# Kernel tuning notes

Hardware: AMD Instinct MI355X
Metric: run time of the kernel (lower is better)

Reference implementation:

```python
import jax, jax.numpy as jnp
import numpy as np

B, N, T, D, H, L, N_HOP = 8, 512, 64, 256, 256, 2, 1
NEG = -1e18


def setup_inputs() -> dict:
    key = jax.random.key(0)
    ks = jax.random.split(key, 16)
    sc = 0.05
    return {
        "attn_mem": jax.random.normal(ks[0], (B, N, D), jnp.float32),
        "mem_sizes": jax.random.randint(ks[1], (B,), 1, N + 1).astype(jnp.int32),
        "lstm_in": jax.random.normal(ks[2], (B, T, D), jnp.float32),
        "init_h": jax.random.uniform(ks[3], (L, H), jnp.float32, -0.01, 0.01),
        "init_c": jax.random.uniform(ks[4], (L, H), jnp.float32, -0.01, 0.01),
        "init_i": jax.random.uniform(ks[5], (D,), jnp.float32, -0.1, 0.1),
        # stacked LSTM weights (layer0 input dim D == H so stacking is valid)
        "w_ih": jax.random.normal(ks[6], (L, 4 * H, D), jnp.float32) * sc,
        "w_hh": jax.random.normal(ks[7], (L, 4 * H, H), jnp.float32) * sc,
        "b_ih": jnp.zeros((L, 4 * H), jnp.float32),
        "b_hh": jnp.zeros((L, 4 * H), jnp.float32),
        "attn_wm": jax.random.normal(ks[8], (D, H), jnp.float32) * sc,
        "attn_wq": jax.random.normal(ks[9], (H, H), jnp.float32) * sc,
        "attn_v": jax.random.uniform(ks[10], (H,), jnp.float32, -0.01, 0.01),
        "hop_wm": jax.random.normal(ks[11], (D, H), jnp.float32) * sc,
        "hop_wq": jax.random.normal(ks[12], (H, H), jnp.float32) * sc,
        "hop_v": jax.random.uniform(ks[13], (H,), jnp.float32, -0.01, 0.01),
    }


def _additive_score(feat, query, v, wq):
    # feat: [B,N,H]  query: [B,S,H]  ->  score: [B,S,N]
    q = query @ wq  # [B,S,H]
    s = jnp.tanh(feat[:, None, :, :] + q[:, :, None, :])  # [B,S,N,H] (large)
    return jnp.einsum("bsnh,h->bsn", s, v)


def _run_lstm(x, h0, c0, w_ih, w_hh, b_ih, b_hh):
    # x: [S,B,D] time-major; PyTorch gate order i,f,g,o
    n_layer = h0.shape[0]

    def step(carry, x_t):
        h, c = carry
        inp = x_t
        hs, cs = [], []
        for l in range(n_layer):
            g = inp @ w_ih[l].T + h[l] @ w_hh[l].T + b_ih[l] + b_hh[l]
            i_g, f_g, g_g, o_g = jnp.split(g, 4, axis=-1)
            c_n = jax.nn.sigmoid(f_g) * c[l] + jax.nn.sigmoid(i_g) * jnp.tanh(g_g)
            h_n = jax.nn.sigmoid(o_g) * jnp.tanh(c_n)
            hs.append(h_n)
            cs.append(c_n)
            inp = h_n
        return (jnp.stack(hs), jnp.stack(cs)), inp

    _, ys = jax.lax.scan(step, (h0, c0), x)
    return ys  # [S,B,H]


def reference(attn_mem, mem_sizes, lstm_in, init_h, init_c, init_i,
              w_ih, w_hh, b_ih, b_hh,
              attn_wm, attn_wq, attn_v, hop_wm, hop_wq, hop_v):
    bs, n_mem, _ = attn_mem.shape
    attn_feat = attn_mem @ attn_wm  # [B,N,H]
    hop_feat = attn_mem @ hop_wm    # [B,N,H]

    h0 = jnp.broadcast_to(init_h[:, None, :], (init_h.shape[0], bs, init_h.shape[1]))
    c0 = jnp.broadcast_to(init_c[:, None, :], h0.shape)
    seq = jnp.concatenate(
        [jnp.broadcast_to(init_i[None, None, :], (bs, 1, init_i.shape[0])), lstm_in],
        axis=1,
    )  # [B,T+1,D]
    query = _run_lstm(seq.transpose(1, 0, 2), h0, c0, w_ih, w_hh, b_ih, b_hh)
    query = query.transpose(1, 0, 2)  # [B,T+1,H]

    valid = jnp.arange(n_mem)[None, None, :] < mem_sizes[:, None, None]  # [B,1,N]
    for _ in range(N_HOP):
        score = _additive_score(hop_feat, query, hop_v, hop_wq)  # [B,T+1,N]
        score = jnp.where(valid, score, NEG)
        norm = jax.nn.softmax(score, axis=-1)
        query = jnp.einsum("bsn,bnh->bsh", norm, hop_feat)

    return _additive_score(attn_feat, query, attn_v, attn_wq)  # [B,T+1,N]
```

## Files before the change

kernel.cpp:

```cpp
#include <hip/hip_runtime.h>

#define BB 8
#define NN 512
#define TT 64
#define SS 65
#define DD 256
#define HH 256
#define G4 1024

__device__ __forceinline__ float fsigmoid(float x) {
    return __builtin_amdgcn_rcpf(1.f + __expf(-x));
}
__device__ __forceinline__ float ftanh(float x) {
    float e = __expf(2.f * x);
    return fmaf(-2.f, __builtin_amdgcn_rcpf(e + 1.f), 1.f);
}

__global__ void prep_kernel(const float* __restrict__ lstm_in,
                            const float* __restrict__ init_i,
                            const float* __restrict__ init_h,
                            float* __restrict__ seq,
                            unsigned long long* __restrict__ S0,
                            unsigned long long* __restrict__ S1) {
    int idx = blockIdx.x * 256 + threadIdx.x;
    if (idx < BB * SS * DD) {
        int d = idx & 255;
        int r = idx >> 8;
        int s = r % SS, b = r / SS;
        seq[idx] = (s == 0) ? init_i[d]
                            : lstm_in[((size_t)b * TT + (s - 1)) * DD + d];
    } else {
        int i = idx - BB * SS * DD;
        if (i < 2048) {
            S0[i] = (1ULL << 32) | (unsigned)__float_as_uint(init_h[i & 255]);
        } else if (i < 4096) {
            S1[i - 2048] = (1ULL << 32) | (unsigned)__float_as_uint(init_h[HH + (i & 255)]);
        } else if (i < 4096 + 65 * 2048) {
            S0[2048 + (i - 4096)] = 0ULL;
        } else {
            S1[2048 + (i - (4096 + 65 * 2048))] = 0ULL;
        }
    }
}

__global__ void __launch_bounds__(256) mega_gemm_kernel(
    const float* __restrict__ attn_mem, const float* __restrict__ attn_wm,
    const float* __restrict__ hop_wm, float* __restrict__ attn_feat,
    float* __restrict__ hop_feat, const float* __restrict__ seq,
    const float* __restrict__ w_ih, const float* __restrict__ b_ih,
    const float* __restrict__ b_hh, float* __restrict__ xg0)
{
    __shared__ float As[16][68];
    __shared__ float Bs[16][68];
    __shared__ float Bs2[16][68];
    const int tid = threadIdx.x;
    const int tm = (tid >> 4) * 4, tn = (tid & 15) * 4;
    const int arow = tid >> 2, akq = (tid & 3) << 2;

    if (blockIdx.x < 256) {
        const int bm = (blockIdx.x & 63) * 64, bn = (blockIdx.x >> 6) * 64;
        float acc1[4][4] = {}, acc2[4][4] = {};
        for (int k0 = 0; k0 < 256; k0 += 16) {
            float4 va = *(const float4*)(attn_mem + (size_t)(bm + arow) * 256 + k0 + akq);
            As[akq + 0][arow] = va.x; As[akq + 1][arow] = va.y;
            As[akq + 2][arow] = va.z; As[akq + 3][arow] = va.w;
            int kk = tid >> 4, nq = (tid & 15) << 2;
            *(float4*)&Bs[kk][nq]  = *(const float4*)(attn_wm + (size_t)(k0 + kk) * 256 + bn + nq);
            *(float4*)&Bs2[kk][nq] = *(const float4*)(hop_wm  + (size_t)(k0 + kk) * 256 + bn + nq);
            __syncthreads();
#pragma unroll
            for (int kk2 = 0; kk2 < 16; ++kk2) {
                float4 a  = *(const float4*)&As[kk2][tm];
                float4 b1 = *(const float4*)&Bs[kk2][tn];
                float4 b2 = *(const float4*)&Bs2[kk2][tn];
                float av[4] = {a.x, a.y, a.z, a.w};
                float b1v[4] = {b1.x, b1.y, b1.z, b1.w};
                float b2v[4] = {b2.x, b2.y, b2.z, b2.w};
#pragma unroll
                for (int i = 0; i < 4; ++i)
#pragma unroll
                    for (int jj = 0; jj < 4; ++jj) {
                        acc1[i][jj] = fmaf(av[i], b1v[jj], acc1[i][jj]);
                        acc2[i][jj] = fmaf(av[i], b2v[jj], acc2[i][jj]);
                    }
            }
            __syncthreads();
        }
#pragma unroll
        for (int i = 0; i < 4; ++i) {
            int m = bm + tm + i;
            *(float4*)(attn_feat + (size_t)m * 256 + bn + tn) =
                make_float4(acc1[i][0], acc1[i][1], acc1[i][2], acc1[i][3]);
            *(float4*)(hop_feat + (size_t)m * 256 + bn + tn) =
                make_float4(acc2[i][0], acc2[i][1], acc2[i][2], acc2[i][3]);
        }
    } else {
        const int blk2 = blockIdx.x - 256;
        const int bm = (blk2 % 9) * 64, bn = (blk2 / 9) * 64;
        float acc[4][4] = {};
        for (int k0 = 0; k0 < 256; k0 += 16) {
            {
                int m = bm + arow;
                float4 v = make_float4(0.f, 0.f, 0.f, 0.f);
                if (m < 520) v = *(const float4*)(seq + (size_t)m * 256 + k0 + akq);
                As[akq + 0][arow] = v.x; As[akq + 1][arow] = v.y;
                As[akq + 2][arow] = v.z; As[akq + 3][arow] = v.w;
            }
            {
                int n = bn + arow;
                float4 v = *(const float4*)(w_ih + (size_t)n * 256 + k0 + akq);
                Bs[akq + 0][n - bn] = v.x; Bs[akq + 1][n - bn] = v.y;
                Bs[akq + 2][n - bn] = v.z; Bs[akq + 3][n - bn] = v.w;
            }
            __syncthreads();
#pragma unroll
            for (int kk2 = 0; kk2 < 16; ++kk2) {
                float4 a = *(const float4*)&As[kk2][tm];
                float4 b = *(const float4*)&Bs[kk2][tn];
                float av[4] = {a.x, a.y, a.z, a.w};
                float bv[4] = {b.x, b.y, b.z, b.w};
#pragma unroll
                for (int i = 0; i < 4; ++i)
#pragma unroll
                    for (int jj = 0; jj < 4; ++jj)
                        acc[i][jj] = fmaf(av[i], bv[jj], acc[i][jj]);
            }
            __syncthreads();
        }
        float bad[4];
#pragma unroll
        for (int jj = 0; jj < 4; ++jj)
            bad[jj] = b_ih[bn + tn + jj] + b_hh[bn + tn + jj];
#pragma unroll
        for (int i = 0; i < 4; ++i) {
            int m = bm + tm + i;
            if (m < 520)
                *(float4*)(xg0 + (size_t)m * 1024 + bn + tn) =
                    make_float4(acc[i][0] + bad[0], acc[i][1] + bad[1],
                                acc[i][2] + bad[2], acc[i][3] + bad[3]);
        }
    }
}

__global__ void gemm_kernel(const float* __restrict__ A, const float* __restrict__ B,
                            float* __restrict__ C, int M, int N, int K) {
    __shared__ float As[16][68];
    __shared__ float Bs[16][68];
    const int tid = threadIdx.x;
    const int bm = blockIdx.x * 64, bn = blockIdx.y * 64;
    const int tm = (tid >> 4) * 4, tn = (tid & 15) * 4;
    const int arow = tid >> 2, akq = (tid & 3) << 2;
    float acc[4][4] = {};
    for (int k0 = 0; k0 < K; k0 += 16) {
        {
            int m = bm + arow;
            float4 v = make_float4(0.f, 0.f, 0.f, 0.f);
            if (m < M) v = *(const float4*)(A + (size_t)m * K + k0 + akq);
            As[akq + 0][arow] = v.x; As[akq + 1][arow] = v.y;
            As[akq + 2][arow] = v.z; As[akq + 3][arow] = v.w;
        }
        {
            int kk = tid >> 4, nq = (tid & 15) << 2;
            float4 v = *(const float4*)(B + (size_t)(k0 + kk) * N + bn + nq);
            *(float4*)&Bs[kk][nq] = v;
        }
        __syncthreads();
#pragma unroll
        for (int kk2 = 0; kk2 < 16; ++kk2) {
            float4 a = *(const float4*)&As[kk2][tm];
            float4 b = *(const float4*)&Bs[kk2][tn];
            float av[4] = {a.x, a.y, a.z, a.w};
            float bv[4] = {b.x, b.y, b.z, b.w};
#pragma unroll
            for (int i = 0; i < 4; ++i)
#pragma unroll
                for (int jj = 0; jj < 4; ++jj)
                    acc[i][jj] = fmaf(av[i], bv[jj], acc[i][jj]);
        }
        __syncthreads();
    }
#pragma unroll
    for (int i = 0; i < 4; ++i) {
        int m = bm + tm + i;
        if (m < M)
            *(float4*)(C + (size_t)m * N + bn + tn) =
                make_float4(acc[i][0], acc[i][1], acc[i][2], acc[i][3]);
    }
}

__device__ __forceinline__ float dot16(const float4* w, const float* hp) {
    float4 s = make_float4(0.f, 0.f, 0.f, 0.f);
#pragma unroll
    for (int k = 0; k < 16; ++k) {
        float4 h4 = *(const float4*)(hp + 4 * k);
        s.x = fmaf(w[k].x, h4.x, s.x);
        s.y = fmaf(w[k].y, h4.y, s.y);
        s.z = fmaf(w[k].z, h4.z, s.z);
        s.w = fmaf(w[k].w, h4.w, s.w);
    }
    return (s.x + s.y) + (s.z + s.w);
}

__device__ __forceinline__ float poll_h(const unsigned long long* p, unsigned want) {
    unsigned long long u = __hip_atomic_load(p, __ATOMIC_RELAXED, __HIP_MEMORY_SCOPE_AGENT);
    while ((unsigned)(u >> 32) != want) {
        __builtin_amdgcn_s_sleep(1);
        u = __hip_atomic_load(p, __ATOMIC_RELAXED, __HIP_MEMORY_SCOPE_AGENT);
    }
    return __uint_as_float((unsigned)u);
}

__global__ void __launch_bounds__(1024, 4) lstm_kernel(
    const float* __restrict__ w_ih, const float* __restrict__ w_hh,
    const float* __restrict__ b_ih, const float* __restrict__ b_hh,
    const float* __restrict__ xg0, const float* __restrict__ init_c,
    unsigned long long* __restrict__ S0, unsigned long long* __restrict__ S1,
    float* __restrict__ query)
{
    __shared__ float hls[64 * 68];
    __shared__ float part[1024];
    const int tid = threadIdx.x;
    const int blk = blockIdx.x;
    const int g = tid * 2;
    const int sb = g >> 8, r0 = g & 255, sg0 = r0 >> 6, kq = r0 & 63;
    float* const dst = &hls[(sg0 * 8 + sb) * 68 + kq];

    if (blk < 32) {
        const int jl = tid & 7, gate = (tid >> 3) & 3, b = (tid >> 5) & 7, seg = tid >> 8;
        const int j0 = blk * 8, j = j0 + jl;
        float4 w[16];
        {
            const float4* wr = (const float4*)(w_hh + (size_t)(gate * HH + j) * HH + seg * 64);
#pragma unroll
            for (int k = 0; k < 16; ++k) w[k] = wr[k];
        }
        const int fj = tid >> 3, fb = tid & 7;
        float creg = (tid < 64) ? init_c[j0 + fj] : 0.f;
        const int chunk = seg * 8 + b;
        const int pidx = (chunk * 8 + jl) * 4 + gate;

        for (int t = 0; t < SS; ++t) {
            float xg[4];
            if (tid < 64) {
                const float* xp = xg0 + ((size_t)fb * SS + t) * G4 + (j0 + fj);
#pragma unroll
                for (int gg = 0; gg < 4; ++gg) xg[gg] = xp[gg * 256];
            }
            {
                const unsigned long long* src = S0 + (size_t)t * 2048 + g;
                dst[0] = poll_h(src, (unsigned)(t + 1));
                dst[1] = poll_h(src + 1, (unsigned)(t + 1));
            }
            __syncthreads();
            part[pidx] = dot16(w, &hls[chunk * 68]);
            __syncthreads();
            if (tid < 64) {
                float g0 = xg[0], g1 = xg[1], g2 = xg[2], g3 = xg[3];
#pragma unroll
                for (int s2 = 0; s2 < 4; ++s2) {
                    const float* pp = &part[((s2 * 8 + fb) * 8 + fj) * 4];
                    g0 += pp[0]; g1 += pp[1]; g2 += pp[2]; g3 += pp[3];
                }
                float c = fsigmoid(g1) * creg + fsigmoid(g0) * ftanh(g2);
                float h = fsigmoid(g3) * ftanh(c);
                creg = c;
                unsigned long long u = ((unsigned long long)(unsigned)(t + 2) << 32)
                                     | (unsigned long long)(unsigned)__float_as_uint(h);
                __hip_atomic_store(S0 + (size_t)(t + 1) * 2048 + fb * 256 + (j0 + fj), u,
                                   __ATOMIC_RELAXED, __HIP_MEMORY_SCOPE_AGENT);
            }
        }
    } else {
        const int jl = tid & 3, gate = (tid >> 2) & 3, b = (tid >> 4) & 7, seg = tid >> 7;
        const int j0 = (blk - 32) * 4, j = j0 + jl;
        float4 w[16];
        {
            const float* base = (seg < 4)
                ? (w_ih + (size_t)(G4 + gate * HH + j) * HH + seg * 64)
                : (w_hh + (size_t)(G4 + gate * HH + j) * HH + (seg - 4) * 64);
            const float4* wr = (const float4*)base;
#pragma unroll
            for (int k = 0; k < 16; ++k) w[k] = wr[k];
        }
        const int fj = tid >> 3, fb = tid & 7;
        float creg = 0.f, bias[4] = {0.f, 0.f, 0.f, 0.f};
        if (tid < 32) {
            creg = init_c[HH + j0 + fj];
#pragma unroll
            for (int gg = 0; gg < 4; ++gg)
                bias[gg] = b_ih[G4 + gg * HH + j0 + fj] + b_hh[G4 + gg * HH + j0 + fj];
        }
        const int chunk = seg * 8 + b;
        const int pidx = chunk * 16 + jl * 4 + gate;

        for (int t = 0; t < SS; ++t) {
            {
                const unsigned long long* src = S0 + (size_t)(t + 1) * 2048 + g;
                dst[0] = poll_h(src, (unsigned)(t + 2));
                dst[1] = poll_h(src + 1, (unsigned)(t + 2));
            }
            __syncthreads();
            if (seg < 4) part[pidx] = dot16(w, &hls[chunk * 68]);
            {
                const unsigned long long* src = S1 + (size_t)t * 2048 + g;
                float v0 = poll_h(src, (unsigned)(t + 1));
                float v1 = poll_h(src + 1, (unsigned)(t + 1));
                dst[32 * 68 + 0] = v0;
                dst[32 * 68 + 1] = v1;
            }
            __syncthreads();
            if (seg >= 4) part[pidx] = dot16(w, &hls[chunk * 68]);
            __syncthreads();
            if (tid < 32) {
                float g0 = bias[0], g1 = bias[1], g2 = bias[2], g3 = bias[3];
#pragma unroll
                for (int s2 = 0; s2 < 8; ++s2) {
                    const float* pp = &part[(s2 * 8 + fb) * 16 + fj * 4];
                    g0 += pp[0]; g1 += pp[1]; g2 += pp[2]; g3 += pp[3];
                }
                float c = fsigmoid(g1) * creg + fsigmoid(g0) * ftanh(g2);
                float h = fsigmoid(g3) * ftanh(c);
                creg = c;
                int jj = j0 + fj;
                unsigned long long u = ((unsigned long long)(unsigned)(t + 2) << 32)
                                     | (unsigned long long)(unsigned)__float_as_uint(h);
                __hip_atomic_store(S1 + (size_t)(t + 1) * 2048 + fb * 256 + jj, u,
                                   __ATOMIC_RELAXED, __HIP_MEMORY_SCOPE_AGENT);
                query[((size_t)fb * SS + t) * HH + jj] = h;
            }
        }
    }
}

__global__ void score_kernel(const float* __restrict__ feat, const float* __restrict__ q,
                             const float* __restrict__ v, const int* __restrict__ mem_sizes,
                             float* __restrict__ out, int masked) {
    const int s = blockIdx.x, b = blockIdx.y;
    __shared__ float qs[256], vs[256];
    const int tid = threadIdx.x;
    qs[tid] = q[((size_t)b * SS + s) * HH + tid];
    vs[tid] = v[tid];
    __syncthreads();
    const int lane = tid & 63, wv = tid >> 6;
    const int msize = masked ? mem_sizes[b] : NN;
    const float* fb = feat + (size_t)b * NN * HH + (lane << 2);
    float* ob = out + ((size_t)b * SS + s) * NN;
    for (int n = msize + tid; n < NN; n += 256) ob[n] = -1e18f;
    float4 q4 = *(const float4*)&qs[lane << 2];
    float4 v4 = *(const float4*)&vs[lane << 2];
    int n = wv;
    for (; n + 4 < msize; n += 8) {
        float4 fa = *(const float4*)(fb + (size_t)n * HH);
        float4 fc = *(const float4*)(fb + (size_t)(n + 4) * HH);
        float a0 = ftanh(fa.x + q4.x) * v4.x + ftanh(fa.y + q4.y) * v4.y
                 + ftanh(fa.z + q4.z) * v4.z + ftanh(fa.w + q4.w) * v4.w;
        float a1 = ftanh(fc.x + q4.x) * v4.x + ftanh(fc.y + q4.y) * v4.y
                 + ftanh(fc.z + q4.z) * v4.z + ftanh(fc.w + q4.w) * v4.w;
#pragma unroll
        for (int off = 32; off; off >>= 1) {
            a0 += __shfl_xor(a0, off, 64);
            a1 += __shfl_xor(a1, off, 64);
        }
        if (lane == 0) { ob[n] = a0; ob[n + 4] = a1; }
    }
    for (; n < msize; n += 4) {
        float4 fa = *(const float4*)(fb + (size_t)n * HH);
        float a0 = ftanh(fa.x + q4.x) * v4.x + ftanh(fa.y + q4.y) * v4.y
                 + ftanh(fa.z + q4.z) * v4.z + ftanh(fa.w + q4.w) * v4.w;
#pragma unroll
        for (int off = 32; off; off >>= 1) a0 += __shfl_xor(a0, off, 64);
        if (lane == 0) ob[n] = a0;
    }
}

__global__ void swsum_kernel(const float* __restrict__ score, const float* __restrict__ feat,
                             const int* __restrict__ mem_sizes, float* __restrict__ out) {
    const int b = blockIdx.y, s0 = blockIdx.x * 5;
    const int tid = threadIdx.x;
    __shared__ float ns[5][512];
    for (int i = tid; i < 5 * 512; i += 256)
        ns[i >> 9][i & 511] = score[((size_t)b * SS + s0 + (i >> 9)) * NN + (i & 511)];
    __syncthreads();
    const int wv = tid >> 6, lane = tid & 63;
    for (int r2 = wv; r2 < 5; r2 += 4) {
        float vv[8];
#pragma unroll
        for (int k = 0; k < 8; ++k) vv[k] = ns[r2][lane + 64 * k];
        float m = vv[0];
#pragma unroll
        for (int k = 1; k < 8; ++k) m = fmaxf(m, vv[k]);
#pragma unroll
        for (int off = 32; off; off >>= 1) m = fmaxf(m, __shfl_xor(m, off, 64));
        float l = 0.f;
#pragma unroll
        for (int k = 0; k < 8; ++k) { vv[k] = __expf(vv[k] - m); l += vv[k]; }
#pragma unroll
        for (int off = 32; off; off >>= 1) l += __shfl_xor(l, off, 64);
        float inv = __builtin_amdgcn_rcpf(l);
#pragma unroll
        for (int k = 0; k < 8; ++k) ns[r2][lane + 64 * k] = vv[k] * inv;
    }
    __syncthreads();
    const int msize = mem_sizes[b];
    const int nmax = (msize + 3) & ~3;
    float a0 = 0.f, a1 = 0.f, a2 = 0.f, a3 = 0.f, a4 = 0.f;
    const float* fb = feat + (size_t)b * NN * HH + tid;
    for (int n = 0; n < nmax; n += 4) {
        float f0 = fb[(size_t)(n + 0) * HH];
        float f1 = fb[(size_t)(n + 1) * HH];
        float f2 = fb[(size_t)(n + 2) * HH];
        float f3 = fb[(size_t)(n + 3) * HH];
        a0 += ns[0][n] * f0 + ns[0][n + 1] * f1 + ns[0][n + 2] * f2 + ns[0][n + 3] * f3;
        a1 += ns[1][n] * f0 + ns[1][n + 1] * f1 + ns[1][n + 2] * f2 + ns[1][n + 3] * f3;
        a2 += ns[2][n] * f0 + ns[2][n + 1] * f1 + ns[2][n + 2] * f2 + ns[2][n + 3] * f3;
        a3 += ns[3][n] * f0 + ns[3][n + 1] * f1 + ns[3][n + 2] * f2 + ns[3][n + 3] * f3;
        a4 += ns[4][n] * f0 + ns[4][n + 1] * f1 + ns[4][n + 2] * f2 + ns[4][n + 3] * f3;
    }
    out[((size_t)b * SS + s0 + 0) * HH + tid] = a0;
    out[((size_t)b * SS + s0 + 1) * HH + tid] = a1;
    out[((size_t)b * SS + s0 + 2) * HH + tid] = a2;
    out[((size_t)b * SS + s0 + 3) * HH + tid] = a3;
    out[((size_t)b * SS + s0 + 4) * HH + tid] = a4;
}

extern "C" void kernel_launch(void* const* d_in, const int* in_sizes, int n_in,
                              void* d_out, int out_size, void* d_ws, size_t ws_size,
                              hipStream_t stream) {
    const float* attn_mem  = (const float*)d_in[0];
    const int*   mem_sizes = (const int*)d_in[1];
    const float* lstm_in   = (const float*)d_in[2];
    const float* init_h    = (const float*)d_in[3];
    const float* init_c    = (const float*)d_in[4];
    const float* init_i    = (const float*)d_in[5];
    const float* w_ih      = (const float*)d_in[6];
    const float* w_hh      = (const float*)d_in[7];
    const float* b_ih      = (const float*)d_in[8];
    const float* b_hh      = (const float*)d_in[9];
    const float* attn_wm   = (const float*)d_in[10];
    const float* attn_wq   = (const float*)d_in[11];
    const float* attn_v    = (const float*)d_in[12];
    const float* hop_wm    = (const float*)d_in[13];
    const float* hop_wq    = (const float*)d_in[14];
    const float* hop_v     = (const float*)d_in[15];
    float* out = (float*)d_out;

    float* ws        = (float*)d_ws;
    float* attn_feat = ws;
    float* hop_feat  = ws + 1048576;
    float* seq       = ws + 2097152;
    float* xg0       = ws + 2230272;
    float* query     = ws + 2762752;
    unsigned long long* S0 = (unsigned long long*)(ws + 2895872);
    unsigned long long* S1 = (unsigned long long*)(ws + 3166208);
    float* q1        = ws + 2895872;
    float* score     = ws + 3028992;
    float* query2    = ws + 3295232;
    float* q2        = ws + 3428352;

    prep_kernel<<<1576, 256, 0, stream>>>(lstm_in, init_i, init_h, seq, S0, S1);
    mega_gemm_kernel<<<400, 256, 0, stream>>>(attn_mem, attn_wm, hop_wm, attn_feat,
                                              hop_feat, seq, w_ih, b_ih, b_hh, xg0);
    {
        void* args[] = { (void*)&w_ih, (void*)&w_hh, (void*)&b_ih, (void*)&b_hh,
                         (void*)&xg0, (void*)&init_c, (void*)&S0, (void*)&S1,
                         (void*)&query };
        hipLaunchCooperativeKernel(lstm_kernel, dim3(96), dim3(1024), args, 0u, stream);
    }
    gemm_kernel<<<dim3(9, 4), 256, 0, stream>>>(query, hop_wq, q1, 520, 256, 256);
    score_kernel<<<dim3(65, 8), 256, 0, stream>>>(hop_feat, q1, hop_v, mem_sizes, score, 1);
    swsum_kernel<<<dim3(13, 8), 256, 0, stream>>>(score, hop_feat, mem_sizes, query2);
    gemm_kernel<<<dim3(9, 4), 256, 0, stream>>>(query2, attn_wq, q2, 520, 256, 256);
    score_kernel<<<dim3(65, 8), 256, 0, stream>>>(attn_feat, q2, attn_v, mem_sizes, out, 0);
}
```

Before: 346.2 us.

## Fuse prep into GEMM kernel, batch score over five queries, remove poll sleep

```diff
diff --git a/kernel.cpp b/kernel.cpp
--- a/kernel.cpp
+++ b/kernel.cpp
@@ -16,63 +16,107 @@
     return fmaf(-2.f, __builtin_amdgcn_rcpf(e + 1.f), 1.f);
 }
 
-__global__ void prep_kernel(const float* __restrict__ lstm_in,
-                            const float* __restrict__ init_i,
-                            const float* __restrict__ init_h,
-                            float* __restrict__ seq,
-                            unsigned long long* __restrict__ S0,
-                            unsigned long long* __restrict__ S1) {
-    int idx = blockIdx.x * 256 + threadIdx.x;
-    if (idx < BB * SS * DD) {
-        int d = idx & 255;
-        int r = idx >> 8;
-        int s = r % SS, b = r / SS;
-        seq[idx] = (s == 0) ? init_i[d]
-                            : lstm_in[((size_t)b * TT + (s - 1)) * DD + d];
-    } else {
-        int i = idx - BB * SS * DD;
+__global__ void __launch_bounds__(256) pre_kernel(
+    const float* __restrict__ lstm_in, const float* __restrict__ init_i,
+    const float* __restrict__ init_h, const float* __restrict__ w_ih,
+    const float* __restrict__ b_ih, const float* __restrict__ b_hh,
+    float* __restrict__ xg0,
+    const float* __restrict__ attn_mem, const float* __restrict__ attn_wm,
+    const float* __restrict__ hop_wm,
+    float* __restrict__ attn_feat, float* __restrict__ hop_feat,
+    unsigned long long* __restrict__ S0, unsigned long long* __restrict__ S1)
+{
+    const int tid = threadIdx.x;
+    const int blk = blockIdx.x;
+    if (blk >= 400) {
+        int i = (blk - 400) * 256 + tid;
         if (i < 2048) {
-            S0[i] = (1ULL << 32) | (unsigned)__float_as_uint(init_h[i & 255]);
+            S0[i] = (1ULL << 32) | (unsigned long long)(unsigned)__float_as_uint(init_h[i & 255]);
         } else if (i < 4096) {
-            S1[i - 2048] = (1ULL << 32) | (unsigned)__float_as_uint(init_h[HH + (i & 255)]);
+            S1[i - 2048] = (1ULL << 32)
+                         | (unsigned long long)(unsigned)__float_as_uint(init_h[HH + (i & 255)]);
         } else if (i < 4096 + 65 * 2048) {
             S0[2048 + (i - 4096)] = 0ULL;
-        } else {
+        } else if (i < 4096 + 130 * 2048) {
             S1[2048 + (i - (4096 + 65 * 2048))] = 0ULL;
         }
-    }
-}
-
-__global__ void __launch_bounds__(256) mega_gemm_kernel(
-    const float* __restrict__ attn_mem, const float* __restrict__ attn_wm,
-    const float* __restrict__ hop_wm, float* __restrict__ attn_feat,
-    float* __restrict__ hop_feat, const float* __restrict__ seq,
-    const float* __restrict__ w_ih, const float* __restrict__ b_ih,
-    const float* __restrict__ b_hh, float* __restrict__ xg0)
-{
-    __shared__ float As[16][68];
-    __shared__ float Bs[16][68];
-    __shared__ float Bs2[16][68];
-    const int tid = threadIdx.x;
+        return;
+    }
+    __shared__ __align__(16) float smem[3264];
     const int tm = (tid >> 4) * 4, tn = (tid & 15) * 4;
     const int arow = tid >> 2, akq = (tid & 3) << 2;
 
-    if (blockIdx.x < 256) {
-        const int bm = (blockIdx.x & 63) * 64, bn = (blockIdx.x >> 6) * 64;
+    if (blk < 144) {
+        float* As = smem;
+        float* Bs = smem + 1088;
+        const int bm = (blk % 9) * 64, bn = (blk / 9) * 64;
+        float acc[4][4] = {};
+        for (int k0 = 0; k0 < 256; k0 += 16) {
+            {
+                int m = bm + arow;
+                float4 v = make_float4(0.f, 0.f, 0.f, 0.f);
+                if (m < 520) {
+                    int s = m % 65, b = m / 65;
+                    const float* src = (s == 0) ? (init_i + k0 + akq)
+                        : (lstm_in + ((size_t)b * TT + (s - 1)) * DD + k0 + akq);
+                    v = *(const float4*)src;
+                }
+                As[(akq + 0) * 68 + arow] = v.x; As[(akq + 1) * 68 + arow] = v.y;
+                As[(akq + 2) * 68 + arow] = v.z; As[(akq + 3) * 68 + arow] = v.w;
+            }
+            {
+                int n = bn + arow;
+                float4 v = *(const float4*)(w_ih + (size_t)n * 256 + k0 + akq);
+                Bs[(akq + 0) * 68 + (n - bn)] = v.x; Bs[(akq + 1) * 68 + (n - bn)] = v.y;
+                Bs[(akq + 2) * 68 + (n - bn)] = v.z; Bs[(akq + 3) * 68 + (n - bn)] = v.w;
+            }
+            __syncthreads();
+#pragma unroll
+            for (int kk = 0; kk < 16; ++kk) {
+                float4 a = *(const float4*)&As[kk * 68 + tm];
+                float4 b = *(const float4*)&Bs[kk * 68 + tn];
+                float av[4] = {a.x, a.y, a.z, a.w};
+                float bv[4] = {b.x, b.y, b.z, b.w};
+#pragma unroll
+                for (int i = 0; i < 4; ++i)
+#pragma unroll
+                    for (int jj = 0; jj < 4; ++jj)
+                        acc[i][jj] = fmaf(av[i], bv[jj], acc[i][jj]);
+            }
+            __syncthreads();
+        }
+        float bad[4];
+#pragma unroll
+        for (int jj = 0; jj < 4; ++jj)
+            bad[jj] = b_ih[bn + tn + jj] + b_hh[bn + tn + jj];
+#pragma unroll
+        for (int i = 0; i < 4; ++i) {
+            int m = bm + tm + i;
+            if (m < 520)
+                *(float4*)(xg0 + (size_t)m * 1024 + bn + tn) =
+                    make_float4(acc[i][0] + bad[0], acc[i][1] + bad[1],
+                                acc[i][2] + bad[2], acc[i][3] + bad[3]);
+        }
+    } else {
+        float* As  = smem;
+        float* Bs  = smem + 1088;
+        float* Bs2 = smem + 2176;
+        const int tileid = blk - 144;
+        const int bm = (tileid & 63) * 64, bn = (tileid >> 6) * 64;
         float acc1[4][4] = {}, acc2[4][4] = {};
         for (int k0 = 0; k0 < 256; k0 += 16) {
             float4 va = *(const float4*)(attn_mem + (size_t)(bm + arow) * 256 + k0 + akq);
-            As[akq + 0][arow] = va.x; As[akq + 1][arow] = va.y;
-            As[akq + 2][arow] = va.z; As[akq + 3][arow] = va.w;
+            As[(akq + 0) * 68 + arow] = va.x; As[(akq + 1) * 68 + arow] = va.y;
+            As[(akq + 2) * 68 + arow] = va.z; As[(akq + 3) * 68 + arow] = va.w;
             int kk = tid >> 4, nq = (tid & 15) << 2;
-            *(float4*)&Bs[kk][nq]  = *(const float4*)(attn_wm + (size_t)(k0 + kk) * 256 + bn + nq);
-            *(float4*)&Bs2[kk][nq] = *(const float4*)(hop_wm  + (size_t)(k0 + kk) * 256 + bn + nq);
+            *(float4*)&Bs[kk * 68 + nq]  = *(const float4*)(attn_wm + (size_t)(k0 + kk) * 256 + bn + nq);
+            *(float4*)&Bs2[kk * 68 + nq] = *(const float4*)(hop_wm  + (size_t)(k0 + kk) * 256 + bn + nq);
             __syncthreads();
 #pragma unroll
             for (int kk2 = 0; kk2 < 16; ++kk2) {
-                float4 a  = *(const float4*)&As[kk2][tm];
-                float4 b1 = *(const float4*)&Bs[kk2][tn];
-                float4 b2 = *(const float4*)&Bs2[kk2][tn];
+                float4 a  = *(const float4*)&As[kk2 * 68 + tm];
+                float4 b1 = *(const float4*)&Bs[kk2 * 68 + tn];
+                float4 b2 = *(const float4*)&Bs2[kk2 * 68 + tn];
                 float av[4] = {a.x, a.y, a.z, a.w};
                 float b1v[4] = {b1.x, b1.y, b1.z, b1.w};
                 float b2v[4] = {b2.x, b2.y, b2.z, b2.w};
@@ -94,97 +138,6 @@
             *(float4*)(hop_feat + (size_t)m * 256 + bn + tn) =
                 make_float4(acc2[i][0], acc2[i][1], acc2[i][2], acc2[i][3]);
         }
-    } else {
-        const int blk2 = blockIdx.x - 256;
-        const int bm = (blk2 % 9) * 64, bn = (blk2 / 9) * 64;
-        float acc[4][4] = {};
-        for (int k0 = 0; k0 < 256; k0 += 16) {
-            {
-                int m = bm + arow;
-                float4 v = make_float4(0.f, 0.f, 0.f, 0.f);
-                if (m < 520) v = *(const float4*)(seq + (size_t)m * 256 + k0 + akq);
-                As[akq + 0][arow] = v.x; As[akq + 1][arow] = v.y;
-                As[akq + 2][arow] = v.z; As[akq + 3][arow] = v.w;
-            }
-            {
-                int n = bn + arow;
-                float4 v = *(const float4*)(w_ih + (size_t)n * 256 + k0 + akq);
-                Bs[akq + 0][n - bn] = v.x; Bs[akq + 1][n - bn] = v.y;
-                Bs[akq + 2][n - bn] = v.z; Bs[akq + 3][n - bn] = v.w;
-            }
-            __syncthreads();
-#pragma unroll
-            for (int kk2 = 0; kk2 < 16; ++kk2) {
-                float4 a = *(const float4*)&As[kk2][tm];
-                float4 b = *(const float4*)&Bs[kk2][tn];
-                float av[4] = {a.x, a.y, a.z, a.w};
-                float bv[4] = {b.x, b.y, b.z, b.w};
-#pragma unroll
-                for (int i = 0; i < 4; ++i)
-#pragma unroll
-                    for (int jj = 0; jj < 4; ++jj)
-                        acc[i][jj] = fmaf(av[i], bv[jj], acc[i][jj]);
-            }
-            __syncthreads();
-        }
-        float bad[4];
-#pragma unroll
-        for (int jj = 0; jj < 4; ++jj)
-            bad[jj] = b_ih[bn + tn + jj] + b_hh[bn + tn + jj];
-#pragma unroll
-        for (int i = 0; i < 4; ++i) {
-            int m = bm + tm + i;
-            if (m < 520)
-                *(float4*)(xg0 + (size_t)m * 1024 + bn + tn) =
-                    make_float4(acc[i][0] + bad[0], acc[i][1] + bad[1],
-                                acc[i][2] + bad[2], acc[i][3] + bad[3]);
-        }
-    }
-}
-
-__global__ void gemm_kernel(const float* __restrict__ A, const float* __restrict__ B,
-                            float* __restrict__ C, int M, int N, int K) {
-    __shared__ float As[16][68];
-    __shared__ float Bs[16][68];
-    const int tid = threadIdx.x;
-    const int bm = blockIdx.x * 64, bn = blockIdx.y * 64;
-    const int tm = (tid >> 4) * 4, tn = (tid & 15) * 4;
-    const int arow = tid >> 2, akq = (tid & 3) << 2;
-    float acc[4][4] = {};
-    for (int k0 = 0; k0 < K; k0 += 16) {
-        {
-            int m = bm + arow;
-            float4 v = make_float4(0.f, 0.f, 0.f, 0.f);
-            if (m < M) v = *(const float4*)(A + (size_t)m * K + k0 + akq);
-            As[akq + 0][arow] = v.x; As[akq + 1][arow] = v.y;
-            As[akq + 2][arow] = v.z; As[akq + 3][arow] = v.w;
-        }
-        {
-            int kk = tid >> 4, nq = (tid & 15) << 2;
-            float4 v = *(const float4*)(B + (size_t)(k0 + kk) * N + bn + nq);
-            *(float4*)&Bs[kk][nq] = v;
-        }
-        __syncthreads();
-#pragma unroll
-        for (int kk2 = 0; kk2 < 16; ++kk2) {
-            float4 a = *(const float4*)&As[kk2][tm];
-            float4 b = *(const float4*)&Bs[kk2][tn];
-            float av[4] = {a.x, a.y, a.z, a.w};
-            float bv[4] = {b.x, b.y, b.z, b.w};
-#pragma unroll
-            for (int i = 0; i < 4; ++i)
-#pragma unroll
-                for (int jj = 0; jj < 4; ++jj)
-                    acc[i][jj] = fmaf(av[i], bv[jj], acc[i][jj]);
-        }
-        __syncthreads();
-    }
-#pragma unroll
-    for (int i = 0; i < 4; ++i) {
-        int m = bm + tm + i;
-        if (m < M)
-            *(float4*)(C + (size_t)m * N + bn + tn) =
-                make_float4(acc[i][0], acc[i][1], acc[i][2], acc[i][3]);
     }
 }
 
@@ -204,7 +157,6 @@
 __device__ __forceinline__ float poll_h(const unsigned long long* p, unsigned want) {
     unsigned long long u = __hip_atomic_load(p, __ATOMIC_RELAXED, __HIP_MEMORY_SCOPE_AGENT);
     while ((unsigned)(u >> 32) != want) {
-        __builtin_amdgcn_s_sleep(1);
         u = __hip_atomic_load(p, __ATOMIC_RELAXED, __HIP_MEMORY_SCOPE_AGENT);
     }
     return __uint_as_float((unsigned)u);
@@ -332,49 +284,108 @@
     }
 }
 
-__global__ void score_kernel(const float* __restrict__ feat, const float* __restrict__ q,
-                             const float* __restrict__ v, const int* __restrict__ mem_sizes,
-                             float* __restrict__ out, int masked) {
-    const int s = blockIdx.x, b = blockIdx.y;
-    __shared__ float qs[256], vs[256];
+__global__ void __launch_bounds__(256) gemm_kernel(
+    const float* __restrict__ A, const float* __restrict__ B,
+    float* __restrict__ C, int M, int N, int K)
+{
+    __shared__ __align__(16) float As[16 * 68];
+    __shared__ __align__(16) float Bs[16 * 68];
     const int tid = threadIdx.x;
-    qs[tid] = q[((size_t)b * SS + s) * HH + tid];
+    const int bm = blockIdx.x * 64, bn = blockIdx.y * 64;
+    const int tm = (tid >> 4) * 4, tn = (tid & 15) * 4;
+    const int arow = tid >> 2, akq = (tid & 3) << 2;
+    float acc[4][4] = {};
+    for (int k0 = 0; k0 < K; k0 += 16) {
+        {
+            int m = bm + arow;
+            float4 v = make_float4(0.f, 0.f, 0.f, 0.f);
+            if (m < M) v = *(const float4*)(A + (size_t)m * K + k0 + akq);
+            As[(akq + 0) * 68 + arow] = v.x; As[(akq + 1) * 68 + arow] = v.y;
+            As[(akq + 2) * 68 + arow] = v.z; As[(akq + 3) * 68 + arow] = v.w;
+        }
+        {
+            int kk = tid >> 4, nq = (tid & 15) << 2;
+            *(float4*)&Bs[kk * 68 + nq] = *(const float4*)(B + (size_t)(k0 + kk) * N + bn + nq);
+        }
+        __syncthreads();
+#pragma unroll
+        for (int kk2 = 0; kk2 < 16; ++kk2) {
+            float4 a = *(const float4*)&As[kk2 * 68 + tm];
+            float4 b = *(const float4*)&Bs[kk2 * 68 + tn];
+            float av[4] = {a.x, a.y, a.z, a.w};
+            float bv[4] = {b.x, b.y, b.z, b.w};
+#pragma unroll
+            for (int i = 0; i < 4; ++i)
+#pragma unroll
+                for (int jj = 0; jj < 4; ++jj)
+                    acc[i][jj] = fmaf(av[i], bv[jj], acc[i][jj]);
+        }
+        __syncthreads();
+    }
+#pragma unroll
+    for (int i = 0; i < 4; ++i) {
+        int m = bm + tm + i;
+        if (m < M)
+            *(float4*)(C + (size_t)m * N + bn + tn) =
+                make_float4(acc[i][0], acc[i][1], acc[i][2], acc[i][3]);
+    }
+}
+
+__global__ void __launch_bounds__(256) score5_kernel(
+    const float* __restrict__ feat, const float* __restrict__ q,
+    const float* __restrict__ v, const int* __restrict__ mem_sizes,
+    float* __restrict__ out, int masked)
+{
+    const int nt = blockIdx.x, st = blockIdx.y, b = blockIdx.z;
+    const int tid = threadIdx.x;
+    const int s0 = st * 5;
+    const int n0 = nt * 256;
+    __shared__ float qs[5][256], vs[256];
     vs[tid] = v[tid];
+#pragma unroll
+    for (int k = 0; k < 5; ++k)
+        qs[k][tid] = q[((size_t)b * SS + s0 + k) * HH + tid];
     __syncthreads();
+    const int msize = masked ? mem_sizes[b] : NN;
+    float* ob = out + ((size_t)b * SS + s0) * NN;
+    if (masked) {
+        int n = n0 + tid;
+        if (n >= msize) {
+#pragma unroll
+            for (int k = 0; k < 5; ++k) ob[(size_t)k * NN + n] = -1e18f;
+        }
+    }
     const int lane = tid & 63, wv = tid >> 6;
-    const int msize = masked ? mem_sizes[b] : NN;
+    float4 v4 = *(const float4*)&vs[lane << 2];
+    float4 q4[5];
+#pragma unroll
+    for (int k = 0; k < 5; ++k) q4[k] = *(const float4*)&qs[k][lane << 2];
     const float* fb = feat + (size_t)b * NN * HH + (lane << 2);
-    float* ob = out + ((size_t)b * SS + s) * NN;
-    for (int n = msize + tid; n < NN; n += 256) ob[n] = -1e18f;
-    float4 q4 = *(const float4*)&qs[lane << 2];
-    float4 v4 = *(const float4*)&vs[lane << 2];
-    int n = wv;
-    for (; n + 4 < msize; n += 8) {
-        float4 fa = *(const float4*)(fb + (size_t)n * HH);
-        float4 fc = *(const float4*)(fb + (size_t)(n + 4) * HH);
-        float a0 = ftanh(fa.x + q4.x) * v4.x + ftanh(fa.y + q4.y) * v4.y
-                 + ftanh(fa.z + q4.z) * v4.z + ftanh(fa.w + q4.w) * v4.w;
-        float a1 = ftanh(fc.x + q4.x) * v4.x + ftanh(fc.y + q4.y) * v4.y
-                 + ftanh(fc.z + q4.z) * v4.z + ftanh(fc.w + q4.w) * v4.w;
+    const int nend = (msize < n0 + 256) ? msize : (n0 + 256);
+    for (int n = n0 + wv; n < nend; n += 4) {
+        float4 f4 = *(const float4*)(fb + (size_t)n * HH);
+        float a[5];
+#pragma unroll
+        for (int k = 0; k < 5; ++k) {
+            a[k] = ftanh(f4.x + q4[k].x) * v4.x + ftanh(f4.y + q4[k].y) * v4.y
+                 + ftanh(f4.z + q4[k].z) * v4.z + ftanh(f4.w + q4[k].w) * v4.w;
+        }
 #pragma unroll
         for (int off = 32; off; off >>= 1) {
-            a0 += __shfl_xor(a0, off, 64);
-            a1 += __shfl_xor(a1, off, 64);
-        }
-        if (lane == 0) { ob[n] = a0; ob[n + 4] = a1; }
-    }
-    for (; n < msize; n += 4) {
-        float4 fa = *(const float4*)(fb + (size_t)n * HH);
-        float a0 = ftanh(fa.x + q4.x) * v4.x + ftanh(fa.y + q4.y) * v4.y
-                 + ftanh(fa.z + q4.z) * v4.z + ftanh(fa.w + q4.w) * v4.w;
-#pragma unroll
-        for (int off = 32; off; off >>= 1) a0 += __shfl_xor(a0, off, 64);
-        if (lane == 0) ob[n] = a0;
-    }
-}
-
-__global__ void swsum_kernel(const float* __restrict__ score, const float* __restrict__ feat,
-                             const int* __restrict__ mem_sizes, float* __restrict__ out) {
+#pragma unroll
+            for (int k = 0; k < 5; ++k) a[k] += __shfl_xor(a[k], off, 64);
+        }
+        if (lane == 0) {
+#pragma unroll
+            for (int k = 0; k < 5; ++k) ob[(size_t)k * NN + n] = a[k];
+        }
+    }
+}
+
+__global__ void __launch_bounds__(256) swsum_kernel(
+    const float* __restrict__ score, const float* __restrict__ feat,
+    const int* __restrict__ mem_sizes, float* __restrict__ out)
+{
     const int b = blockIdx.y, s0 = blockIdx.x * 5;
     const int tid = threadIdx.x;
     __shared__ float ns[5][512];
@@ -447,19 +458,19 @@
     float* ws        = (float*)d_ws;
     float* attn_feat = ws;
     float* hop_feat  = ws + 1048576;
-    float* seq       = ws + 2097152;
-    float* xg0       = ws + 2230272;
-    float* query     = ws + 2762752;
-    unsigned long long* S0 = (unsigned long long*)(ws + 2895872);
-    unsigned long long* S1 = (unsigned long long*)(ws + 3166208);
-    float* q1        = ws + 2895872;
-    float* score     = ws + 3028992;
-    float* query2    = ws + 3295232;
-    float* q2        = ws + 3428352;
-
-    prep_kernel<<<1576, 256, 0, stream>>>(lstm_in, init_i, init_h, seq, S0, S1);
-    mega_gemm_kernel<<<400, 256, 0, stream>>>(attn_mem, attn_wm, hop_wm, attn_feat,
-                                              hop_feat, seq, w_ih, b_ih, b_hh, xg0);
+    float* xg0       = ws + 2097152;
+    float* query     = ws + 2629632;
+    float* region    = ws + 2762752;
+    unsigned long long* S0 = (unsigned long long*)region;
+    unsigned long long* S1 = (unsigned long long*)(region + 270336);
+    float* q1     = region;
+    float* sc     = region + 133120;
+    float* q2raw  = region + 399360;
+    float* q2     = region + 532480;
+
+    pre_kernel<<<1456, 256, 0, stream>>>(lstm_in, init_i, init_h, w_ih, b_ih, b_hh,
+                                         xg0, attn_mem, attn_wm, hop_wm,
+                                         attn_feat, hop_feat, S0, S1);
     {
         void* args[] = { (void*)&w_ih, (void*)&w_hh, (void*)&b_ih, (void*)&b_hh,
                          (void*)&xg0, (void*)&init_c, (void*)&S0, (void*)&S1,
@@ -467,8 +478,10 @@
         hipLaunchCooperativeKernel(lstm_kernel, dim3(96), dim3(1024), args, 0u, stream);
     }
     gemm_kernel<<<dim3(9, 4), 256, 0, stream>>>(query, hop_wq, q1, 520, 256, 256);
-    score_kernel<<<dim3(65, 8), 256, 0, stream>>>(hop_feat, q1, hop_v, mem_sizes, score, 1);
-    swsum_kernel<<<dim3(13, 8), 256, 0, stream>>>(score, hop_feat, mem_sizes, query2);
-    gemm_kernel<<<dim3(9, 4), 256, 0, stream>>>(query2, attn_wq, q2, 520, 256, 256);
-    score_kernel<<<dim3(65, 8), 256, 0, stream>>>(attn_feat, q2, attn_v, mem_sizes, out, 0);
-}
+    score5_kernel<<<dim3(2, 13, 8), 256, 0, stream>>>(hop_feat, q1, hop_v,
+                                                      mem_sizes, sc, 1);
+    swsum_kernel<<<dim3(13, 8), 256, 0, stream>>>(sc, hop_feat, mem_sizes, q2raw);
+    gemm_kernel<<<dim3(9, 4), 256, 0, stream>>>(q2raw, attn_wq, q2, 520, 256, 256);
+    score5_kernel<<<dim3(2, 13, 8), 256, 0, stream>>>(attn_feat, q2, attn_v,
+                                                      mem_sizes, out, 0);
+}
```

Result: slower. 393.9 us (+13.8%).
